# Kernel tuning notes

Measured on AMD Instinct MI355X. Metric: run time of the kernel, lower is better.

The kernel has to match this reference:

```python
import jax, jax.numpy as jnp
import numpy as np

B, H, W, D, C = 2, 32, 32, 16, 384
HEADS = 12
WH = WW = WD = 4
NOISE = 256
EPS = 1e-5


def setup_inputs() -> dict:
    key = jax.random.key(0)
    ks = jax.random.split(key, 12)
    s = 0.02
    return {
        "x": jax.random.normal(ks[0], (B, H, W, D, C), jnp.float32),
        "x_noise": jax.random.normal(ks[1], (B, NOISE), jnp.float32),
        "ada_w": jax.random.normal(ks[2], (6 * C, NOISE), jnp.float32) * s,
        "ada_b": jax.random.normal(ks[3], (6 * C,), jnp.float32) * s,
        "qkv_w": jax.random.normal(ks[4], (3 * C, C), jnp.float32) * s,
        "qkv_b": jax.random.normal(ks[5], (3 * C,), jnp.float32) * s,
        "out_w": jax.random.normal(ks[6], (C, C), jnp.float32) * s,
        "out_b": jax.random.normal(ks[7], (C,), jnp.float32) * s,
        "mlp_w1": jax.random.normal(ks[8], (4 * C, C), jnp.float32) * s,
        "mlp_b1": jax.random.normal(ks[9], (4 * C,), jnp.float32) * s,
        "mlp_w2": jax.random.normal(ks[10], (C, 4 * C), jnp.float32) * s,
        "mlp_b2": jax.random.normal(ks[11], (C,), jnp.float32) * s,
    }


def _ln(y):
    # LayerNorm without affine (elementwise_affine=False when use_ada_ln_zero)
    m = jnp.mean(y, axis=-1, keepdims=True)
    v = jnp.mean(jnp.square(y - m), axis=-1, keepdims=True)
    return (y - m) * jax.lax.rsqrt(v + EPS)


def _mod(y, shift, scale):
    # shift/scale: [B, C] broadcast over spatial dims
    return y * (1.0 + scale[:, None, None, None, :]) + shift[:, None, None, None, :]


def _gate(y, g):
    return y * g[:, None, None, None, :]


def _window_attn(q, k, v):
    # q,k,v: [B,H,W,D,C] -> windows [nw, heads, L, hd]
    hd = C // HEADS

    def part(t):
        t = t.reshape(B, H // WH, WH, W // WW, WW, D // WD, WD, HEADS, hd)
        t = t.transpose(0, 1, 3, 5, 7, 2, 4, 6, 8)  # b h w d he wh ww wd hd
        return t.reshape(-1, HEADS, WH * WW * WD, hd)

    q, k, v = part(q), part(k), part(v)
    scores = jnp.einsum("nhlc,nhmc->nhlm", q, k) / jnp.sqrt(jnp.float32(hd))
    attn = jax.nn.softmax(scores, axis=-1)
    o = jnp.einsum("nhlm,nhmc->nhlc", attn, v)
    o = o.reshape(B, H // WH, W // WW, D // WD, HEADS, WH, WW, WD, hd)
    o = o.transpose(0, 1, 5, 2, 6, 3, 7, 4, 8)  # b h wh w ww d wd he hd
    return o.reshape(B, H, W, D, C)


def reference(x, x_noise, ada_w, ada_b, qkv_w, qkv_b, out_w, out_b,
              mlp_w1, mlp_b1, mlp_w2, mlp_b2):
    # AdaLN-Zero params
    params = jax.nn.silu(x_noise) @ ada_w.T + ada_b  # [B, 6C]
    shift1, scale1, gate1, shift2, scale2, gate2 = jnp.split(params, 6, axis=-1)

    # attention branch
    qkv = _mod(_ln(x), shift1, scale1) @ qkv_w.T + qkv_b  # [B,H,W,D,3C]
    q, k, v = jnp.split(qkv, 3, axis=-1)
    attn_out = _window_attn(q, k, v)
    x = x + _gate(attn_out @ out_w.T + out_b, gate1)

    # MLP branch
    h = _mod(_ln(x), shift2, scale2) @ mlp_w1.T + mlp_b1
    h = jax.nn.gelu(h, approximate=False) @ mlp_w2.T + mlp_b2
    return x + _gate(h, gate2)
```

## Files before the change

### kernel.cpp

```cpp
#include <hip/hip_runtime.h>
#include <math.h>

typedef __bf16 bf16;
typedef __attribute__((ext_vector_type(8))) __bf16 bf16x8;
typedef __attribute__((ext_vector_type(4))) float f32x4;

__device__ __forceinline__ bf16 f2bf(float f) {
  union { float f; unsigned u; } a; a.f = f;
  unsigned r = a.u + 0x7fffu + ((a.u >> 16) & 1u);
  union { unsigned short u; bf16 b; } o; o.u = (unsigned short)(r >> 16);
  return o.b;
}

__device__ __forceinline__ void async_load16(const void* g, void* l) {
  __builtin_amdgcn_global_load_lds(
      (const __attribute__((address_space(1))) void*)g,
      (__attribute__((address_space(3))) void*)l, 16, 0, 0);
}

__global__ void f2b4_kernel(const float* __restrict__ a, bf16* __restrict__ oa, int na,
                            const float* __restrict__ b, bf16* __restrict__ ob, int nb,
                            const float* __restrict__ c, bf16* __restrict__ oc, int nc,
                            const float* __restrict__ d, bf16* __restrict__ od, int nd) {
  const int total = na + nb + nc + nd;
  for (int i = blockIdx.x * 256 + threadIdx.x; i < total; i += gridDim.x * 256) {
    const float* s; bf16* o; int j = i;
    if (j < na) { s = a; o = oa; }
    else { j -= na;
      if (j < nb) { s = b; o = ob; }
      else { j -= nb;
        if (j < nc) { s = c; o = oc; }
        else { j -= nc; s = d; o = od; } } }
    o[j] = f2bf(s[j]);
  }
}

__global__ __launch_bounds__(256)
void ada_kernel(const float* __restrict__ xn, const float* __restrict__ aw,
                const float* __restrict__ ab, float* __restrict__ params) {
  const int wid = (blockIdx.x << 2) + (threadIdx.x >> 6);
  const int ln = threadIdx.x & 63;
  const int j = wid % 2304, b = wid / 2304;
  float s = 0.f;
#pragma unroll
  for (int e = 0; e < 4; e++) {
    int idx = ln + (e << 6);
    float x = xn[b * 256 + idx];
    s += (x / (1.f + __expf(-x))) * aw[j * 256 + idx];
  }
#pragma unroll
  for (int m = 1; m < 64; m <<= 1) s += __shfl_xor(s, m);
  if (ln == 0) params[b * 2304 + j] = s + ab[j];
}

__global__ __launch_bounds__(256)
void ln_mod_kernel(const float* __restrict__ xin, const float* __restrict__ params,
                   int so, int co, bf16* __restrict__ y) {
  const int tok = (blockIdx.x << 2) + (threadIdx.x >> 6);
  const int ln = threadIdx.x & 63;
  const float* xr = xin + (size_t)tok * 384;
  float v[6]; float s = 0.f, s2 = 0.f;
#pragma unroll
  for (int e = 0; e < 6; e++) { float x = xr[ln + (e << 6)]; v[e] = x; s += x; s2 += x * x; }
#pragma unroll
  for (int m = 1; m < 64; m <<= 1) { s += __shfl_xor(s, m); s2 += __shfl_xor(s2, m); }
  const float mean = s * (1.f / 384.f);
  const float var = s2 * (1.f / 384.f) - mean * mean;
  const float rs = rsqrtf(var + 1e-5f);
  const int b = tok >> 14;
  const float* pr = params + b * 2304;
  bf16* yr = y + (size_t)tok * 384;
#pragma unroll
  for (int e = 0; e < 6; e++) {
    int c = ln + (e << 6);
    float nv = (v[e] - mean) * rs;
    yr[c] = f2bf(nv * (1.f + pr[co + c]) + pr[so + c]);
  }
}

template<int MODE>
__global__ __launch_bounds__(256)
void gemm_bt(const bf16* __restrict__ A, const bf16* __restrict__ W,
             const float* __restrict__ bias, const float* __restrict__ gate,
             const float* __restrict__ xres, float* __restrict__ outf,
             bf16* __restrict__ outb, int M, int N, int K) {
  __shared__ __align__(16) bf16 As[3][4096];
  __shared__ __align__(16) bf16 Bs[3][4096];
  const int t = threadIdx.x;
  const int ntn = N >> 7;
  int wg = blockIdx.x;
  wg = (wg & 7) * (gridDim.x >> 3) + (wg >> 3);
  const int bm = (wg / ntn) << 7;
  const int bn = (wg % ntn) << 7;
  const int wid = t >> 6, ln = t & 63;
  const int wr = (wid >> 1) << 6, wc = (wid & 1) << 6;
  const int lrow = ln & 15;
  const int rdoff = (((ln >> 4) ^ (lrow & 3) ^ ((lrow >> 2) & 3)) & 3) << 3;

  f32x4 acc[4][4] = {};

  const int srow = t >> 2;
  const int scol = ((((t & 3) ^ (srow & 3) ^ ((srow >> 2) & 3)) & 3) << 3);
  const bf16* ga = A + (size_t)(bm + srow) * K + scol;
  const bf16* gb = W + (size_t)(bn + srow) * K + scol;
  const size_t rowskip = (size_t)64 * K;
  const int nk = K >> 5;

#define STAGE(buf, kt) do { const int k0_ = (kt) << 5;                 \
    async_load16(ga + k0_, &As[buf][t * 8]);                           \
    async_load16(ga + k0_ + rowskip, &As[buf][2048 + t * 8]);          \
    async_load16(gb + k0_, &Bs[buf][t * 8]);                           \
    async_load16(gb + k0_ + rowskip, &Bs[buf][2048 + t * 8]); } while (0)

  STAGE(0, 0); STAGE(1, 1); STAGE(2, 2);
  int cur = 0;
  for (int tk = 0; tk < nk; ++tk) {
    if (tk + 2 < nk)      asm volatile("s_waitcnt vmcnt(8)" ::: "memory");
    else if (tk + 1 < nk) asm volatile("s_waitcnt vmcnt(4)" ::: "memory");
    else                  asm volatile("s_waitcnt vmcnt(0)" ::: "memory");
    asm volatile("s_barrier" ::: "memory");

    bf16x8 af[4], bfr[4];
#pragma unroll
    for (int i = 0; i < 4; i++)
      af[i] = *(const bf16x8*)&As[cur][(wr + i * 16 + lrow) * 32 + rdoff];
#pragma unroll
    for (int j = 0; j < 4; j++)
      bfr[j] = *(const bf16x8*)&Bs[cur][(wc + j * 16 + lrow) * 32 + rdoff];
    asm volatile("s_waitcnt lgkmcnt(0)" ::: "memory");
    __builtin_amdgcn_sched_barrier(0);
    asm volatile("s_barrier" ::: "memory");

    if (tk + 3 < nk) STAGE(cur, tk + 3);

#pragma unroll
    for (int i = 0; i < 4; i++)
#pragma unroll
      for (int j = 0; j < 4; j++)
        acc[i][j] = __builtin_amdgcn_mfma_f32_16x16x32_bf16(af[i], bfr[j], acc[i][j], 0, 0, 0);

    cur = (cur == 2) ? 0 : cur + 1;
  }
#undef STAGE

  const int lr4 = (ln >> 4) << 2;
#pragma unroll
  for (int i = 0; i < 4; i++) {
#pragma unroll
    for (int j = 0; j < 4; j++) {
      const int n = bn + wc + j * 16 + lrow;
      const float bs = bias[n];
#pragma unroll
      for (int r = 0; r < 4; r++) {
        const size_t m = (size_t)(bm + wr + i * 16 + lr4 + r);
        float v = acc[i][j][r] + bs;
        if constexpr (MODE == 0) {
          outb[m * N + n] = f2bf(v);
        } else if constexpr (MODE == 1) {
          float u = 0.7978845608f * (v + 0.044715f * v * v * v);
          float e = __expf(-2.0f * u);
          float th = (1.0f - e) / (1.0f + e);
          v = 0.5f * v * (1.0f + th);
          outb[m * N + n] = f2bf(v);
        } else {
          const float g = gate[(m >> 14) * 2304 + n];
          outf[m * (size_t)N + n] = xres[m * (size_t)N + n] + g * v;
        }
      }
    }
  }
}

__global__ __launch_bounds__(256)
void attn_kernel(const bf16* __restrict__ qkv, bf16* __restrict__ out) {
  __shared__ __align__(16) bf16 Pl[4][64][72];
  __shared__ __align__(16) bf16 Vt[4][32][72];
  const int t = threadIdx.x, wv = t >> 6, ln = t & 63;
  const int blk = blockIdx.x;
  const int win = blk / 3, hg = blk % 3;
  const int head = hg * 4 + wv;
  const int db = win & 3, wb = (win >> 2) & 7, hb = (win >> 5) & 7, b = win >> 8;
  const int base = ((b * 32 + hb * 4) * 32 + wb * 4) * 16 + db * 4;
  const int lrow = ln & 15, lk8 = (ln >> 4) << 3;
  const float scale = 0.17677669529663689f;

#define TOKROW(q) (base + ((q) >> 4) * 512 + (((q) >> 2) & 3) * 16 + ((q) & 3))

  {
    size_t rb = (size_t)TOKROW(ln) * 1152 + 768 + head * 32;
#pragma unroll
    for (int fi = 0; fi < 4; fi++) {
      bf16x8 v = *(const bf16x8*)(qkv + rb + fi * 8);
#pragma unroll
      for (int e = 0; e < 8; e++) Vt[wv][fi * 8 + e][ln] = v[e];
    }
  }

  f32x4 sacc[4][4] = {};
  {
    bf16x8 qf[4], kf[4];
#pragma unroll
    for (int mi = 0; mi < 4; mi++)
      qf[mi] = *(const bf16x8*)(qkv + (size_t)TOKROW(mi * 16 + lrow) * 1152 + head * 32 + lk8);
#pragma unroll
    for (int nj = 0; nj < 4; nj++)
      kf[nj] = *(const bf16x8*)(qkv + (size_t)TOKROW(nj * 16 + lrow) * 1152 + 384 + head * 32 + lk8);
#pragma unroll
    for (int mi = 0; mi < 4; mi++)
#pragma unroll
      for (int nj = 0; nj < 4; nj++)
        sacc[mi][nj] = __builtin_amdgcn_mfma_f32_16x16x32_bf16(qf[mi], kf[nj], sacc[mi][nj], 0, 0, 0);
  }

#pragma unroll
  for (int mi = 0; mi < 4; mi++) {
#pragma unroll
    for (int r = 0; r < 4; r++) {
      float s0 = sacc[mi][0][r] * scale, s1 = sacc[mi][1][r] * scale;
      float s2 = sacc[mi][2][r] * scale, s3 = sacc[mi][3][r] * scale;
      float mx = fmaxf(fmaxf(s0, s1), fmaxf(s2, s3));
#pragma unroll
      for (int m = 1; m < 16; m <<= 1) mx = fmaxf(mx, __shfl_xor(mx, m));
      float e0 = __expf(s0 - mx), e1 = __expf(s1 - mx), e2 = __expf(s2 - mx), e3 = __expf(s3 - mx);
      float sm = e0 + e1 + e2 + e3;
#pragma unroll
      for (int m = 1; m < 16; m <<= 1) sm += __shfl_xor(sm, m);
      const float inv = 1.0f / sm;
      const int row = mi * 16 + ((ln >> 4) << 2) + r;
      Pl[wv][row][0 + lrow]  = f2bf(e0 * inv);
      Pl[wv][row][16 + lrow] = f2bf(e1 * inv);
      Pl[wv][row][32 + lrow] = f2bf(e2 * inv);
      Pl[wv][row][48 + lrow] = f2bf(e3 * inv);
    }
  }

  f32x4 oacc[4][2] = {};
#pragma unroll
  for (int kk = 0; kk < 2; kk++) {
    bf16x8 pa[4], vb[2];
#pragma unroll
    for (int mi = 0; mi < 4; mi++) pa[mi] = *(const bf16x8*)&Pl[wv][mi * 16 + lrow][kk * 32 + lk8];
#pragma unroll
    for (int nj = 0; nj < 2; nj++) vb[nj] = *(const bf16x8*)&Vt[wv][nj * 16 + lrow][kk * 32 + lk8];
#pragma unroll
    for (int mi = 0; mi < 4; mi++)
#pragma unroll
      for (int nj = 0; nj < 2; nj++)
        oacc[mi][nj] = __builtin_amdgcn_mfma_f32_16x16x32_bf16(pa[mi], vb[nj], oacc[mi][nj], 0, 0, 0);
  }

#pragma unroll
  for (int mi = 0; mi < 4; mi++)
#pragma unroll
    for (int nj = 0; nj < 2; nj++)
#pragma unroll
      for (int r = 0; r < 4; r++) {
        int q = mi * 16 + ((ln >> 4) << 2) + r;
        out[(size_t)TOKROW(q) * 384 + head * 32 + nj * 16 + lrow] = f2bf(oacc[mi][nj][r]);
      }
#undef TOKROW
}

extern "C" void kernel_launch(void* const* d_in, const int* in_sizes, int n_in,
                              void* d_out, int out_size, void* d_ws, size_t ws_size,
                              hipStream_t stream) {
  const float* x      = (const float*)d_in[0];
  const float* xnoise = (const float*)d_in[1];
  const float* ada_w  = (const float*)d_in[2];
  const float* ada_b  = (const float*)d_in[3];
  const float* qkv_w  = (const float*)d_in[4];
  const float* qkv_b  = (const float*)d_in[5];
  const float* out_w  = (const float*)d_in[6];
  const float* out_b  = (const float*)d_in[7];
  const float* mlp_w1 = (const float*)d_in[8];
  const float* mlp_b1 = (const float*)d_in[9];
  const float* mlp_w2 = (const float*)d_in[10];
  const float* mlp_b2 = (const float*)d_in[11];
  float* out = (float*)d_out;

  char* ws = (char*)d_ws;
  float* params = (float*)(ws + 0);
  bf16* wq    = (bf16*)(ws + 18432);
  bf16* wo    = (bf16*)(ws + 903168);
  bf16* w1    = (bf16*)(ws + 1198080);
  bf16* w2    = (bf16*)(ws + 2377728);
  bf16* ybuf  = (bf16*)(ws + 3557376);
  bf16* qkvb  = (bf16*)(ws + 28723200);
  bf16* hbuf  = qkvb;

  f2b4_kernel<<<2048, 256, 0, stream>>>(qkv_w, wq, 442368, out_w, wo, 147456,
                                        mlp_w1, w1, 589824, mlp_w2, w2, 589824);
  ada_kernel<<<1152, 256, 0, stream>>>(xnoise, ada_w, ada_b, params);
  ln_mod_kernel<<<8192, 256, 0, stream>>>(x, params, 0, 384, ybuf);
  gemm_bt<0><<<dim3(256 * 9), 256, 0, stream>>>(ybuf, wq, qkv_b, nullptr, nullptr, nullptr,
                                                qkvb, 32768, 1152, 384);
  attn_kernel<<<1536, 256, 0, stream>>>(qkvb, ybuf);
  gemm_bt<2><<<dim3(256 * 3), 256, 0, stream>>>(ybuf, wo, out_b, params + 2 * 384, x, out,
                                                nullptr, 32768, 384, 384);
  ln_mod_kernel<<<8192, 256, 0, stream>>>(out, params, 1152, 1536, ybuf);
  gemm_bt<1><<<dim3(256 * 12), 256, 0, stream>>>(ybuf, w1, mlp_b1, nullptr, nullptr, nullptr,
                                                 hbuf, 32768, 1536, 384);
  gemm_bt<2><<<dim3(256 * 3), 256, 0, stream>>>(hbuf, w2, mlp_b2, params + 5 * 384, out, out,
                                                nullptr, 32768, 384, 1536);

  (void)in_sizes; (void)n_in; (void)out_size; (void)ws_size;
}
```

Baseline: 375.2 us.

## Pre-pack weights into MFMA fragment layout and load B directly to registers

The weight conversion kernel now writes bf16 weights in a fragment-packed layout, so each lane's 8-element MFMA operand sits contiguously. The GEMM then drops the LDS staging of B and loads B fragments straight from global memory into double-buffered registers one k-tile ahead. The main loop is unrolled by two with hand-tuned vmcnt waits and raised priority around the MFMAs. This halves LDS traffic and footprint, which may help occupancy, but B reads now go uncached through LDS and rely on L2 hits. The fixed prologue and epilogue assume nk is at least 4 and even.

```diff
diff --git a/kernel.cpp b/kernel.cpp
--- a/kernel.cpp
+++ b/kernel.cpp
@@ -18,21 +18,29 @@
       (__attribute__((address_space(3))) void*)l, 16, 0, 0);
 }
 
-__global__ void f2b4_kernel(const float* __restrict__ a, bf16* __restrict__ oa, int na,
-                            const float* __restrict__ b, bf16* __restrict__ ob, int nb,
-                            const float* __restrict__ c, bf16* __restrict__ oc, int nc,
-                            const float* __restrict__ d, bf16* __restrict__ od, int nd) {
-  const int total = na + nb + nc + nd;
-  for (int i = blockIdx.x * 256 + threadIdx.x; i < total; i += gridDim.x * 256) {
-    const float* s; bf16* o; int j = i;
-    if (j < na) { s = a; o = oa; }
-    else { j -= na;
-      if (j < nb) { s = b; o = ob; }
-      else { j -= nb;
-        if (j < nc) { s = c; o = oc; }
-        else { j -= nc; s = d; o = od; } } }
-    o[j] = f2bf(s[j]);
-  }
+__global__ __launch_bounds__(256)
+void packw4_kernel(const float* __restrict__ s0, bf16* __restrict__ d0, int n0,
+                   const float* __restrict__ s1, bf16* __restrict__ d1, int n1,
+                   const float* __restrict__ s2, bf16* __restrict__ d2, int n2,
+                   const float* __restrict__ s3, bf16* __restrict__ d3, int n3)
+{
+  int g = blockIdx.x * 256 + threadIdx.x;
+  const float* s; bf16* d; int K;
+  if (g < n0) { s = s0; d = d0; K = 384; }
+  else { g -= n0;
+    if (g < n1) { s = s1; d = d1; K = 384; }
+    else { g -= n1;
+      if (g < n2) { s = s2; d = d2; K = 384; }
+      else { g -= n2; s = s3; d = d3; K = 1536; } } }
+  const int nkt = K >> 5;
+  const int fid = g >> 6, l = g & 63;
+  const int nt = fid / nkt, kt = fid - nt * nkt;
+  const int row = (nt << 4) + (l & 15);
+  const int k = (kt << 5) + ((l >> 4) << 3);
+  const float* sp = s + (size_t)row * K + k;
+  bf16* dp = d + (size_t)g * 8;
+#pragma unroll
+  for (int e = 0; e < 8; e++) dp[e] = f2bf(sp[e]);
 }
 
 __global__ __launch_bounds__(256)
@@ -80,12 +88,11 @@
 
 template<int MODE>
 __global__ __launch_bounds__(256)
-void gemm_bt(const bf16* __restrict__ A, const bf16* __restrict__ W,
+void gemm_bt(const bf16* __restrict__ A, const bf16* __restrict__ Wp,
              const float* __restrict__ bias, const float* __restrict__ gate,
              const float* __restrict__ xres, float* __restrict__ outf,
              bf16* __restrict__ outb, int M, int N, int K) {
   __shared__ __align__(16) bf16 As[3][4096];
-  __shared__ __align__(16) bf16 Bs[3][4096];
   const int t = threadIdx.x;
   const int ntn = N >> 7;
   int wg = blockIdx.x;
@@ -96,52 +103,65 @@
   const int wr = (wid >> 1) << 6, wc = (wid & 1) << 6;
   const int lrow = ln & 15;
   const int rdoff = (((ln >> 4) ^ (lrow & 3) ^ ((lrow >> 2) & 3)) & 3) << 3;
+  const int nk = K >> 5;
 
   f32x4 acc[4][4] = {};
+  bf16x8 bb0[4], bb1[4];
 
   const int srow = t >> 2;
   const int scol = ((((t & 3) ^ (srow & 3) ^ ((srow >> 2) & 3)) & 3) << 3);
   const bf16* ga = A + (size_t)(bm + srow) * K + scol;
-  const bf16* gb = W + (size_t)(bn + srow) * K + scol;
-  const size_t rowskip = (size_t)64 * K;
-  const int nk = K >> 5;
-
-#define STAGE(buf, kt) do { const int k0_ = (kt) << 5;                 \
+  const size_t rs64 = (size_t)64 * K;
+  const bf16* gw = Wp + ((size_t)(((bn + wc) >> 4) * nk) * 64 + (size_t)ln) * 8;
+  const size_t wstride = (size_t)nk * 512;
+
+#define STAGEA(buf, kt) do { const int k0_ = (kt) << 5;                \
     async_load16(ga + k0_, &As[buf][t * 8]);                           \
-    async_load16(ga + k0_ + rowskip, &As[buf][2048 + t * 8]);          \
-    async_load16(gb + k0_, &Bs[buf][t * 8]);                           \
-    async_load16(gb + k0_ + rowskip, &Bs[buf][2048 + t * 8]); } while (0)
-
-  STAGE(0, 0); STAGE(1, 1); STAGE(2, 2);
+    async_load16(ga + k0_ + rs64, &As[buf][2048 + t * 8]); } while (0)
+#define LOADB(BBv, kt) do { _Pragma("unroll") for (int j = 0; j < 4; j++) \
+    BBv[j] = *(const bf16x8*)(gw + (size_t)j * wstride + (size_t)(kt) * 512); } while (0)
+
+#define BODY(TK, BBC, BBL, TOPW, MFW, DOSTAGE, DOB)                            \
+  {                                                                            \
+    asm volatile("s_waitcnt vmcnt(" TOPW ")" ::: "memory");                    \
+    asm volatile("s_barrier" ::: "memory");        \
+    bf16x8 af[4];                                                              \
+    _Pragma("unroll") for (int i = 0; i < 4; i++)                              \
+      af[i] = *(const bf16x8*)&As[cur][(wr + i * 16 + lrow) * 32 + rdoff];     \
+    asm volatile("s_waitcnt lgkmcnt(0)" ::: "memory");                         \
+    __builtin_amdgcn_sched_barrier(0);                            \
+    asm volatile("s_barrier" ::: "memory");        \
+    if (DOB) { LOADB(BBL, (TK) + 1); __builtin_amdgcn_sched_barrier(0); }      \
+    if (DOSTAGE) { STAGEA(cur, (TK) + 3); __builtin_amdgcn_sched_barrier(0); } \
+    asm volatile("s_waitcnt vmcnt(" MFW ")" ::: "memory");    \
+    __builtin_amdgcn_sched_barrier(0);                                         \
+    __builtin_amdgcn_s_setprio(1);                                             \
+    _Pragma("unroll") for (int i = 0; i < 4; i++)                              \
+      _Pragma("unroll") for (int j = 0; j < 4; j++)                            \
+        acc[i][j] = __builtin_amdgcn_mfma_f32_16x16x32_bf16(af[i], BBC[j], acc[i][j], 0, 0, 0); \
+    __builtin_amdgcn_s_setprio(0);                                             \
+    cur = (cur == 2) ? 0 : cur + 1;                                            \
+  }
+
+  STAGEA(0, 0);  __builtin_amdgcn_sched_barrier(0);
+  LOADB(bb0, 0); __builtin_amdgcn_sched_barrier(0);
+  STAGEA(1, 1);  __builtin_amdgcn_sched_barrier(0);
+  STAGEA(2, 2);  __builtin_amdgcn_sched_barrier(0);
   int cur = 0;
-  for (int tk = 0; tk < nk; ++tk) {
-    if (tk + 2 < nk)      asm volatile("s_waitcnt vmcnt(8)" ::: "memory");
-    else if (tk + 1 < nk) asm volatile("s_waitcnt vmcnt(4)" ::: "memory");
-    else                  asm volatile("s_waitcnt vmcnt(0)" ::: "memory");
-    asm volatile("s_barrier" ::: "memory");
-
-    bf16x8 af[4], bfr[4];
-#pragma unroll
-    for (int i = 0; i < 4; i++)
-      af[i] = *(const bf16x8*)&As[cur][(wr + i * 16 + lrow) * 32 + rdoff];
-#pragma unroll
-    for (int j = 0; j < 4; j++)
-      bfr[j] = *(const bf16x8*)&Bs[cur][(wc + j * 16 + lrow) * 32 + rdoff];
-    asm volatile("s_waitcnt lgkmcnt(0)" ::: "memory");
-    __builtin_amdgcn_sched_barrier(0);
-    asm volatile("s_barrier" ::: "memory");
-
-    if (tk + 3 < nk) STAGE(cur, tk + 3);
-
-#pragma unroll
-    for (int i = 0; i < 4; i++)
-#pragma unroll
-      for (int j = 0; j < 4; j++)
-        acc[i][j] = __builtin_amdgcn_mfma_f32_16x16x32_bf16(af[i], bfr[j], acc[i][j], 0, 0, 0);
-
-    cur = (cur == 2) ? 0 : cur + 1;
-  }
-#undef STAGE
+
+  BODY(0, bb0, bb1, "8", "10", true, true);
+  BODY(1, bb1, bb0, "8", "8",  true, true);
+  for (int tk = 2; tk + 5 < nk; tk += 2) {
+    BODY(tk,     bb0, bb1, "12", "8", true, true);
+    BODY(tk + 1, bb1, bb0, "12", "8", true, true);
+  }
+  BODY(nk - 4, bb0, bb1, "12", "8", true,  true);
+  BODY(nk - 3, bb1, bb0, "12", "6", false, true);
+  BODY(nk - 2, bb0, bb1, "10", "4", false, true);
+  BODY(nk - 1, bb1, bb0, "8",  "0", false, false);
+#undef BODY
+#undef LOADB
+#undef STAGEA
 
   const int lr4 = (ln >> 4) << 2;
 #pragma unroll
@@ -288,8 +308,8 @@
   bf16* qkvb  = (bf16*)(ws + 28723200);
   bf16* hbuf  = qkvb;
 
-  f2b4_kernel<<<2048, 256, 0, stream>>>(qkv_w, wq, 442368, out_w, wo, 147456,
-                                        mlp_w1, w1, 589824, mlp_w2, w2, 589824);
+  packw4_kernel<<<864, 256, 0, stream>>>(qkv_w, wq, 55296, out_w, wo, 18432,
+                                         mlp_w1, w1, 73728, mlp_w2, w2, 73728);
   ada_kernel<<<1152, 256, 0, stream>>>(xnoise, ada_w, ada_b, params);
   ln_mod_kernel<<<8192, 256, 0, stream>>>(x, params, 0, 384, ybuf);
   gemm_bt<0><<<dim3(256 * 9), 256, 0, stream>>>(ybuf, wq, qkv_b, nullptr, nullptr, nullptr,
```

Measured after the change: 367.0 us. -2.2%, faster.
